# Optimization experiments

Measured on AMD Instinct MI355X. Metric: run time of the kernel, lower is better.

The kernel has to match this reference:

```python
import jax, jax.numpy as jnp
import numpy as np

DIM = 8          # per-head dim
EPS = 1e-15
GROUPS_PW = 192  # 3 * heads = 3 * 64


def _conv(x, w, groups=1, pad=0):
    return jax.lax.conv_general_dilated(
        x, w, window_strides=(1, 1), padding=[(pad, pad), (pad, pad)],
        dimension_numbers=('NCHW', 'OIHW', 'NCHW'), feature_group_count=groups)


def setup_inputs() -> dict:
    key = jax.random.key(0)
    k0, k1, k2, k3, k4 = jax.random.split(key, 5)
    B, C, H, W = 4, 512, 64, 64
    td = 512  # heads * dim
    x = jax.random.normal(k0, (B, C, H, W), jnp.float32)
    w_qkv = jax.random.normal(k1, (3 * td, C, 1, 1), jnp.float32) * 0.05
    w_dw = jax.random.normal(k2, (3 * td, 1, 5, 5), jnp.float32) * 0.05
    w_pw = jax.random.normal(k3, (3 * td, (3 * td) // GROUPS_PW, 1, 1), jnp.float32) * 0.05
    w_proj = jax.random.normal(k4, (C, 2 * td, 1, 1), jnp.float32) * 0.05
    return {'x': x, 'w_qkv': w_qkv, 'w_dw': w_dw, 'w_pw': w_pw, 'w_proj': w_proj}


def reference(x, w_qkv, w_dw, w_pw, w_proj):
    # qkv projection (1x1 conv, no bias, no norm/act per config)
    qkv = _conv(x, w_qkv)  # [B, 3*td, H, W]
    # multi-scale aggregation: depthwise 5x5 then grouped 1x1 (groups = 3*heads)
    agg = _conv(_conv(qkv, w_dw, groups=w_dw.shape[0], pad=2), w_pw, groups=GROUPS_PW)
    qkv = jnp.concatenate([qkv, agg], axis=1)  # [B, 6*td, H, W]

    B, _, H, W = qkv.shape
    qkv = qkv.reshape(B, -1, 3 * DIM, H * W)  # [B, h_eff, 3*dim, HW]
    q = jax.nn.relu(qkv[:, :, :DIM])          # [B, h, dim, HW]
    k = jax.nn.relu(qkv[:, :, DIM:2 * DIM])   # [B, h, dim, HW]
    v = qkv[:, :, 2 * DIM:]                   # [B, h, dim, HW]
    # pad v with a row of ones -> normalization trick
    v = jnp.pad(v, ((0, 0), (0, 0), (0, 1), (0, 0)), constant_values=1.0)
    # linear attention via associativity: (v k^T) q
    vk = jnp.einsum('bhdn,bhen->bhde', v, k)   # [B, h, dim+1, dim]
    out = jnp.einsum('bhde,bhen->bhdn', vk, q) # [B, h, dim+1, HW]
    out = out[:, :, :-1] / (out[:, :, -1:] + EPS)
    out = out.reshape(B, -1, H, W)             # [B, 2*td, H, W]
    return x + _conv(out, w_proj)
```

## Files before the change

### kernel.cpp

```cpp
#include <hip/hip_runtime.h>
#include <hip/hip_bf16.h>
#include <cstdint>
#include <cstddef>


typedef __hip_bfloat16 bf16;
typedef __attribute__((ext_vector_type(8))) short short8;
typedef __attribute__((ext_vector_type(4))) float f32x4;

__device__ __forceinline__ float b2f(bf16 v) { return __bfloat162float(v); }
__device__ __forceinline__ bf16 f2b(float v) { return __float2bfloat16(v); }

__device__ __forceinline__ void async16(void* lds_base, const void* gaddr) {
    __builtin_amdgcn_global_load_lds(
        (const __attribute__((address_space(1))) unsigned int*)gaddr,
        (__attribute__((address_space(3))) unsigned int*)lds_base,
        16, 0, 0);
}

__global__ __launch_bounds__(256) void convert_kernel(
    const float* __restrict__ src, bf16* __restrict__ dst, int n)
{
    int i = blockIdx.x * 256 + threadIdx.x;
    if (i < n) dst[i] = f2b(src[i]);
}

__global__ __launch_bounds__(256) void transpose_x_kernel(
    const float* __restrict__ x, bf16* __restrict__ x_t)
{
    __shared__ bf16 tile[32][33];
    const int b = blockIdx.z;
    const int c0 = blockIdx.y * 32;
    const int n0 = blockIdx.x * 32;
    const int tx = threadIdx.x & 31, ty = threadIdx.x >> 5;
    #pragma unroll
    for (int i = 0; i < 32; i += 8)
        tile[ty + i][tx] = f2b(x[((size_t)b * 512 + c0 + ty + i) * 4096 + n0 + tx]);
    __syncthreads();
    #pragma unroll
    for (int i = 0; i < 32; i += 8)
        x_t[((size_t)b * 4096 + n0 + ty + i) * 512 + c0 + tx] = tile[tx][ty + i];
}

template <bool PROJ>
__global__ __launch_bounds__(256) void mfma_gemm_kernel(
    const bf16* __restrict__ A, const bf16* __restrict__ xt_or_qkv,
    const bf16* __restrict__ agg, const float* __restrict__ X,
    void* __restrict__ Cout, int M, int K)
{
    constexpr int N = 4096;
    const int b = blockIdx.z;
    const int m_blk = blockIdx.y * 128;
    const int n_blk = blockIdx.x * 128;

    __shared__ short As[128 * 32];
    __shared__ short Bs[128 * 32];

    const int tid = threadIdx.x;
    const int lane = tid & 63, wave = tid >> 6;
    const int wm = (wave >> 1) * 64, wn = (wave & 1) * 64;
    const int fm = lane & 15, fq = lane >> 4;

    f32x4 acc[4][4] = {};

    const short* Ag = (const short*)A;
    const short* Btg = PROJ ? nullptr
        : (const short*)(xt_or_qkv + (size_t)b * N * 512);

    for (int k0 = 0; k0 < K; k0 += 32) {
        #pragma unroll
        for (int t0 = 0; t0 < 2; ++t0) {
            int t = wave + t0 * 4;
            int row = m_blk + t * 16 + (lane >> 2);
            int col = k0 + (lane & 3) * 8;
            async16(&As[t * 512], Ag + (size_t)row * K + col);
        }
        #pragma unroll
        for (int t0 = 0; t0 < 2; ++t0) {
            int t = wave + t0 * 4;
            int n = n_blk + t * 16 + (lane >> 2);
            if (!PROJ) {
                int col = k0 + (lane & 3) * 8;
                async16(&Bs[t * 512], Btg + (size_t)n * 512 + col);
            } else {
                int h = (k0 >> 3) + (lane & 3);
                const bf16* chunk = (h < 64 ? xt_or_qkv : agg) +
                    ((size_t)b * 1536 + (size_t)(h & 63) * 24 + 16) * 4096;
                async16(&Bs[t * 512], chunk + (size_t)n * 8);
            }
        }
        __syncthreads();

        short8 af[4], bfv[4];
        #pragma unroll
        for (int i = 0; i < 4; ++i)
            af[i] = *(const short8*)&As[(wm + i * 16 + fm) * 32 + fq * 8];
        #pragma unroll
        for (int j = 0; j < 4; ++j)
            bfv[j] = *(const short8*)&Bs[(wn + j * 16 + fm) * 32 + fq * 8];
        #pragma unroll
        for (int i = 0; i < 4; ++i)
            #pragma unroll
            for (int j = 0; j < 4; ++j)
                acc[i][j] = __builtin_amdgcn_mfma_f32_16x16x32_bf16(
                    af[i], bfv[j], acc[i][j], 0, 0, 0);
        __syncthreads();
    }

    if (!PROJ) {
        bf16* Cb = (bf16*)Cout + (size_t)b * M * N;
        #pragma unroll
        for (int i = 0; i < 4; ++i)
            #pragma unroll
            for (int j = 0; j < 4; ++j) {
                int n = n_blk + wn + j * 16 + fm;
                #pragma unroll
                for (int r = 0; r < 4; ++r) {
                    int m = m_blk + wm + i * 16 + fq * 4 + r;
                    Cb[(size_t)m * N + n] = f2b(acc[i][j][r]);
                }
            }
    } else {
        float* Ob = (float*)Cout + (size_t)b * M * N;
        const float* Xb = X + (size_t)b * M * N;
        #pragma unroll
        for (int i = 0; i < 4; ++i)
            #pragma unroll
            for (int j = 0; j < 4; ++j) {
                int n = n_blk + wn + j * 16 + fm;
                #pragma unroll
                for (int r = 0; r < 4; ++r) {
                    int m = m_blk + wm + i * 16 + fq * 4 + r;
                    size_t off = (size_t)m * N + n;
                    Ob[off] = acc[i][j][r] + Xb[off];
                }
            }
    }
}

__global__ __launch_bounds__(256) void dwpw_kernel(
    const bf16* __restrict__ qkv, const float* __restrict__ w_dw,
    const float* __restrict__ w_pw, bf16* __restrict__ agg)
{
    const int bg = blockIdx.y;
    const int b = bg / 192;
    const int g = bg - b * 192;
    const int y0 = blockIdx.x * 16;

    __shared__ float s_in[8][20][68];
    __shared__ float s_wdw[8][28];
    __shared__ float s_wpw[8][8];

    const int tid = threadIdx.x;

    if (tid < 200) {
        int c = tid / 25, k = tid - c * 25;
        s_wdw[c][k] = w_dw[(size_t)(g * 8 + c) * 25 + k];
    }
    if (tid < 64)
        s_wpw[tid >> 3][tid & 7] = w_pw[(size_t)(g * 8 + (tid >> 3)) * 8 + (tid & 7)];

    if (tid < 160) {
        int c = tid / 20, r = tid - c * 20;
        float* row = &s_in[c][r][0];
        row[0] = 0.f; row[1] = 0.f; row[66] = 0.f; row[67] = 0.f;
    }

    const size_t chan_base = ((size_t)b * 1536 + g * 8) * 4096;

    #pragma unroll
    for (int it = 0; it < 5; ++it) {
        int tk = it * 256 + tid;
        int c = tk / 160;
        int rem = tk - c * 160;
        int r = rem >> 3;
        int ck = rem & 7;
        int y = y0 + r - 2;
        float f[8];
        if (y >= 0 && y < 64) {
            short8 raw = *(const short8*)(qkv + chan_base + (size_t)c * 4096
                                          + (size_t)y * 64 + ck * 8);
            #pragma unroll
            for (int d = 0; d < 8; ++d)
                f[d] = __uint_as_float(((unsigned)(unsigned short)raw[d]) << 16);
        } else {
            #pragma unroll
            for (int d = 0; d < 8; ++d) f[d] = 0.f;
        }
        float* dst = &s_in[c][r][2 + ck * 8];
        #pragma unroll
        for (int q = 0; q < 4; ++q)
            *(float2*)(dst + 2 * q) = make_float2(f[2 * q], f[2 * q + 1]);
    }
    __syncthreads();

    const int py = tid >> 4;
    const int px = (tid & 15) * 4;

    float dwv[8][4];
    #pragma unroll
    for (int c = 0; c < 8; ++c) {
        float w[25];
        #pragma unroll
        for (int q = 0; q < 6; ++q)
            *(float4*)&w[q * 4] = *(const float4*)&s_wdw[c][q * 4];
        w[24] = s_wdw[c][24];

        float a0 = 0.f, a1 = 0.f, a2 = 0.f, a3 = 0.f;
        #pragma unroll
        for (int i = 0; i < 5; ++i) {
            const float* row = &s_in[c][py + i][px];
            float4 f0 = *(const float4*)row;
            float4 f1 = *(const float4*)(row + 4);
            float f[8] = {f0.x, f0.y, f0.z, f0.w, f1.x, f1.y, f1.z, f1.w};
            #pragma unroll
            for (int j = 0; j < 5; ++j) {
                float wi = w[i * 5 + j];
                a0 += f[j]     * wi;
                a1 += f[j + 1] * wi;
                a2 += f[j + 2] * wi;
                a3 += f[j + 3] * wi;
            }
        }
        dwv[c][0] = a0; dwv[c][1] = a1; dwv[c][2] = a2; dwv[c][3] = a3;
    }

    const size_t out_pix = (size_t)(y0 + py) * 64 + px;
    #pragma unroll
    for (int o = 0; o < 8; ++o) {
        float wv[8];
        *(float4*)&wv[0] = *(const float4*)&s_wpw[o][0];
        *(float4*)&wv[4] = *(const float4*)&s_wpw[o][4];
        float s0 = 0.f, s1 = 0.f, s2 = 0.f, s3 = 0.f;
        #pragma unroll
        for (int i = 0; i < 8; ++i) {
            s0 += dwv[i][0] * wv[i];
            s1 += dwv[i][1] * wv[i];
            s2 += dwv[i][2] * wv[i];
            s3 += dwv[i][3] * wv[i];
        }
        union { bf16 hv[4]; uint2 u; } pk;
        pk.hv[0] = f2b(s0); pk.hv[1] = f2b(s1);
        pk.hv[2] = f2b(s2); pk.hv[3] = f2b(s3);
        *(uint2*)(agg + chan_base + (size_t)o * 4096 + out_pix) = pk.u;
    }
}

__global__ __launch_bounds__(256) void vk_kernel(
    const bf16* __restrict__ qkv, const bf16* __restrict__ agg,
    float* __restrict__ vk)
{
    const int bh = blockIdx.x;
    const int b = bh >> 7;
    const int h = bh & 127;
    const bf16* base = (h < 64)
        ? (qkv + ((size_t)b * 1536 + h * 24) * 4096)
        : (agg + ((size_t)b * 1536 + (h - 64) * 24) * 4096);

    const int tid = threadIdx.x;
    float acc[9][8] = {};

    for (int n = tid; n < 4096; n += 256) {
        float kv[8], vv[8];
        #pragma unroll
        for (int e = 0; e < 8; ++e) kv[e] = fmaxf(b2f(base[(size_t)(8 + e) * 4096 + n]), 0.f);
        #pragma unroll
        for (int d = 0; d < 8; ++d) vv[d] = b2f(base[(size_t)(16 + d) * 4096 + n]);
        #pragma unroll
        for (int d = 0; d < 8; ++d)
            #pragma unroll
            for (int e = 0; e < 8; ++e)
                acc[d][e] += vv[d] * kv[e];
        #pragma unroll
        for (int e = 0; e < 8; ++e) acc[8][e] += kv[e];
    }

    __shared__ float red[4][72];
    const int lane = tid & 63, wave = tid >> 6;
    #pragma unroll
    for (int d = 0; d < 9; ++d) {
        #pragma unroll
        for (int e = 0; e < 8; ++e) {
            float v = acc[d][e];
            #pragma unroll
            for (int off = 32; off > 0; off >>= 1) v += __shfl_down(v, off, 64);
            if (lane == 0) red[wave][d * 8 + e] = v;
        }
    }
    __syncthreads();
    if (tid < 72) {
        float v = red[0][tid] + red[1][tid] + red[2][tid] + red[3][tid];
        vk[(size_t)bh * 72 + tid] = v;
    }
}

__global__ __launch_bounds__(256) void attn_out_kernel(
    bf16* __restrict__ qkv, bf16* __restrict__ agg,
    const float* __restrict__ vk)
{
    const int b = blockIdx.z;
    const int h = blockIdx.y;
    const int n = blockIdx.x * 256 + threadIdx.x;
    bf16* base = (h < 64)
        ? (qkv + ((size_t)b * 1536 + h * 24) * 4096)
        : (agg + ((size_t)b * 1536 + (h - 64) * 24) * 4096);

    __shared__ float s_vk[72];
    if (threadIdx.x < 72)
        s_vk[threadIdx.x] = vk[((size_t)b * 128 + h) * 72 + threadIdx.x];
    __syncthreads();

    float q[8];
    #pragma unroll
    for (int e = 0; e < 8; ++e) q[e] = fmaxf(b2f(base[(size_t)e * 4096 + n]), 0.f);

    float o[9];
    #pragma unroll
    for (int d = 0; d < 9; ++d) {
        float s = 0.f;
        #pragma unroll
        for (int e = 0; e < 8; ++e) s += s_vk[d * 8 + e] * q[e];
        o[d] = s;
    }
    const float denom = o[8] + 1e-15f;

    union { bf16 hv[8]; uint4 u; } pk;
    #pragma unroll
    for (int d = 0; d < 8; ++d) pk.hv[d] = f2b(o[d] / denom);
    *(uint4*)((char*)(base + (size_t)16 * 4096) + (size_t)n * 16) = pk.u;
}

extern "C" void kernel_launch(void* const* d_in, const int* in_sizes, int n_in,
                              void* d_out, int out_size, void* d_ws, size_t ws_size,
                              hipStream_t stream) {
    const float* x      = (const float*)d_in[0];
    const float* w_qkv  = (const float*)d_in[1];
    const float* w_dw   = (const float*)d_in[2];
    const float* w_pw   = (const float*)d_in[3];
    const float* w_proj = (const float*)d_in[4];

    char* ws = (char*)d_ws;
    bf16* w_qkv_bf  = (bf16*)ws;
    bf16* w_proj_bf = (bf16*)(ws + 1572864);
    float* vkbf     = (float*)(ws + 1572864 + 1048576);
    bf16* x_t       = (bf16*)(ws + 1572864 + 1048576 + 147456);
    bf16* qkv       = x_t + (size_t)4 * 4096 * 512;
    bf16* agg       = qkv + (size_t)4 * 1536 * 4096;

    convert_kernel<<<3072, 256, 0, stream>>>(w_qkv, w_qkv_bf, 786432);
    convert_kernel<<<2048, 256, 0, stream>>>(w_proj, w_proj_bf, 524288);
    transpose_x_kernel<<<dim3(128, 16, 4), 256, 0, stream>>>(x, x_t);

    mfma_gemm_kernel<false><<<dim3(32, 12, 4), 256, 0, stream>>>(
        w_qkv_bf, x_t, nullptr, nullptr, qkv, 1536, 512);

    dwpw_kernel<<<dim3(4, 768), 256, 0, stream>>>(qkv, w_dw, w_pw, agg);

    vk_kernel<<<dim3(512), 256, 0, stream>>>(qkv, agg, vkbf);

    attn_out_kernel<<<dim3(16, 128, 4), 256, 0, stream>>>(qkv, agg, vkbf);

    mfma_gemm_kernel<true><<<dim3(32, 4, 4), 256, 0, stream>>>(
        w_proj_bf, qkv, agg, x, d_out, 512, 1024);
}
```

Baseline: 274.4 us.

## Store dwpw input tile as bf16 in LDS and compute 8 pixels per thread

The depthwise+pointwise kernel now keeps its halo input tile in LDS as raw bf16 rather than fp32, which halves shared memory use. The block size drops to 128 threads and each thread computes 8 output pixels instead of 4. This gives more register reuse of the loaded window and allows 16-byte output stores. In exchange there are more per-thread registers, a bf16-to-fp32 conversion on every LDS read, and misaligned global reads (row+8*ck-2) during the halo load.

```diff
diff --git a/kernel.cpp b/kernel.cpp
--- a/kernel.cpp
+++ b/kernel.cpp
@@ -6,10 +6,14 @@
 
 typedef __hip_bfloat16 bf16;
 typedef __attribute__((ext_vector_type(8))) short short8;
+typedef __attribute__((ext_vector_type(4))) short short4b;
 typedef __attribute__((ext_vector_type(4))) float f32x4;
 
 __device__ __forceinline__ float b2f(bf16 v) { return __bfloat162float(v); }
 __device__ __forceinline__ bf16 f2b(float v) { return __float2bfloat16(v); }
+__device__ __forceinline__ float us2f(unsigned short u) {
+    return __uint_as_float(((unsigned)u) << 16);
+}
 
 __device__ __forceinline__ void async16(void* lds_base, const void* gaddr) {
     __builtin_amdgcn_global_load_lds(
@@ -138,7 +142,7 @@
     }
 }
 
-__global__ __launch_bounds__(256) void dwpw_kernel(
+__global__ __launch_bounds__(128) void dwpw_kernel(
     const bf16* __restrict__ qkv, const float* __restrict__ w_dw,
     const float* __restrict__ w_pw, bf16* __restrict__ agg)
 {
@@ -147,57 +151,52 @@
     const int g = bg - b * 192;
     const int y0 = blockIdx.x * 16;
 
-    __shared__ float s_in[8][20][68];
+    __shared__ unsigned short s_in[8][20][72];
     __shared__ float s_wdw[8][28];
     __shared__ float s_wpw[8][8];
 
     const int tid = threadIdx.x;
 
-    if (tid < 200) {
-        int c = tid / 25, k = tid - c * 25;
+    for (int i = tid; i < 200; i += 128) {
+        int c = i / 25, k = i - c * 25;
         s_wdw[c][k] = w_dw[(size_t)(g * 8 + c) * 25 + k];
     }
     if (tid < 64)
         s_wpw[tid >> 3][tid & 7] = w_pw[(size_t)(g * 8 + (tid >> 3)) * 8 + (tid & 7)];
 
-    if (tid < 160) {
-        int c = tid / 20, r = tid - c * 20;
-        float* row = &s_in[c][r][0];
-        row[0] = 0.f; row[1] = 0.f; row[66] = 0.f; row[67] = 0.f;
-    }
-
     const size_t chan_base = ((size_t)b * 1536 + g * 8) * 4096;
 
-    #pragma unroll
-    for (int it = 0; it < 5; ++it) {
-        int tk = it * 256 + tid;
-        int c = tk / 160;
-        int rem = tk - c * 160;
-        int r = rem >> 3;
-        int ck = rem & 7;
+    for (int it = 0; it < 12; ++it) {
+        int idx = it * 128 + tid;
+        if (idx >= 1440) break;
+        int c = idx / 180;
+        int rem = idx - c * 180;
+        int r = rem / 9;
+        int ck = rem - r * 9;
         int y = y0 + r - 2;
-        float f[8];
+        unsigned short o[8] = {0, 0, 0, 0, 0, 0, 0, 0};
         if (y >= 0 && y < 64) {
-            short8 raw = *(const short8*)(qkv + chan_base + (size_t)c * 4096
-                                          + (size_t)y * 64 + ck * 8);
-            #pragma unroll
-            for (int d = 0; d < 8; ++d)
-                f[d] = __uint_as_float(((unsigned)(unsigned short)raw[d]) << 16);
-        } else {
-            #pragma unroll
-            for (int d = 0; d < 8; ++d) f[d] = 0.f;
-        }
-        float* dst = &s_in[c][r][2 + ck * 8];
-        #pragma unroll
-        for (int q = 0; q < 4; ++q)
-            *(float2*)(dst + 2 * q) = make_float2(f[2 * q], f[2 * q + 1]);
+            const unsigned short* row =
+                (const unsigned short*)(qkv + chan_base + (size_t)c * 4096 + y * 64);
+            if (ck == 0) {
+                unsigned short t[6];
+                __builtin_memcpy(t, row, 12);
+                #pragma unroll
+                for (int q = 0; q < 6; ++q) o[2 + q] = t[q];
+            } else if (ck == 8) {
+                __builtin_memcpy(o, row + 62, 4);
+            } else {
+                __builtin_memcpy(o, row + 8 * ck - 2, 16);
+            }
+        }
+        __builtin_memcpy(&s_in[c][r][8 * ck], o, 16);
     }
     __syncthreads();
 
-    const int py = tid >> 4;
-    const int px = (tid & 15) * 4;
-
-    float dwv[8][4];
+    const int py = tid >> 3;
+    const int sx = tid & 7;
+
+    float dwv[8][8];
     #pragma unroll
     for (int c = 0; c < 8; ++c) {
         float w[25];
@@ -206,43 +205,43 @@
             *(float4*)&w[q * 4] = *(const float4*)&s_wdw[c][q * 4];
         w[24] = s_wdw[c][24];
 
-        float a0 = 0.f, a1 = 0.f, a2 = 0.f, a3 = 0.f;
+        float a[8] = {};
         #pragma unroll
         for (int i = 0; i < 5; ++i) {
-            const float* row = &s_in[c][py + i][px];
-            float4 f0 = *(const float4*)row;
-            float4 f1 = *(const float4*)(row + 4);
-            float f[8] = {f0.x, f0.y, f0.z, f0.w, f1.x, f1.y, f1.z, f1.w};
+            const unsigned short* rp = &s_in[c][py + i][8 * sx];
+            short8 v0 = *(const short8*)rp;
+            short4b v1 = *(const short4b*)(rp + 8);
+            float f[12];
+            #pragma unroll
+            for (int k = 0; k < 8; ++k) f[k] = us2f((unsigned short)v0[k]);
+            #pragma unroll
+            for (int k = 0; k < 4; ++k) f[8 + k] = us2f((unsigned short)v1[k]);
             #pragma unroll
             for (int j = 0; j < 5; ++j) {
                 float wi = w[i * 5 + j];
-                a0 += f[j]     * wi;
-                a1 += f[j + 1] * wi;
-                a2 += f[j + 2] * wi;
-                a3 += f[j + 3] * wi;
-            }
-        }
-        dwv[c][0] = a0; dwv[c][1] = a1; dwv[c][2] = a2; dwv[c][3] = a3;
-    }
-
-    const size_t out_pix = (size_t)(y0 + py) * 64 + px;
+                #pragma unroll
+                for (int x = 0; x < 8; ++x) a[x] += f[j + x] * wi;
+            }
+        }
+        #pragma unroll
+        for (int x = 0; x < 8; ++x) dwv[c][x] = a[x];
+    }
+
+    const size_t out_pix = (size_t)(y0 + py) * 64 + 8 * sx;
     #pragma unroll
     for (int o = 0; o < 8; ++o) {
         float wv[8];
         *(float4*)&wv[0] = *(const float4*)&s_wpw[o][0];
         *(float4*)&wv[4] = *(const float4*)&s_wpw[o][4];
-        float s0 = 0.f, s1 = 0.f, s2 = 0.f, s3 = 0.f;
-        #pragma unroll
-        for (int i = 0; i < 8; ++i) {
-            s0 += dwv[i][0] * wv[i];
-            s1 += dwv[i][1] * wv[i];
-            s2 += dwv[i][2] * wv[i];
-            s3 += dwv[i][3] * wv[i];
-        }
-        union { bf16 hv[4]; uint2 u; } pk;
-        pk.hv[0] = f2b(s0); pk.hv[1] = f2b(s1);
-        pk.hv[2] = f2b(s2); pk.hv[3] = f2b(s3);
-        *(uint2*)(agg + chan_base + (size_t)o * 4096 + out_pix) = pk.u;
+        float s[8] = {};
+        #pragma unroll
+        for (int i = 0; i < 8; ++i)
+            #pragma unroll
+            for (int x = 0; x < 8; ++x) s[x] += dwv[i][x] * wv[i];
+        union { bf16 hv[8]; uint4 u; } pk;
+        #pragma unroll
+        for (int x = 0; x < 8; ++x) pk.hv[x] = f2b(s[x]);
+        *(uint4*)(agg + chan_base + (size_t)o * 4096 + out_pix) = pk.u;
     }
 }
 
@@ -354,7 +353,7 @@
     mfma_gemm_kernel<false><<<dim3(32, 12, 4), 256, 0, stream>>>(
         w_qkv_bf, x_t, nullptr, nullptr, qkv, 1536, 512);
 
-    dwpw_kernel<<<dim3(4, 768), 256, 0, stream>>>(qkv, w_dw, w_pw, agg);
+    dwpw_kernel<<<dim3(4, 768), 128, 0, stream>>>(qkv, w_dw, w_pw, agg);
 
     vk_kernel<<<dim3(512), 256, 0, stream>>>(qkv, agg, vkbf);
 
```

Result: no change. 272.0 us (-0.9%).
